# Performance work log

Hardware: AMD Instinct MI355X
Metric: run time of the kernel (lower is better)

Reference implementation:

```python
import jax, jax.numpy as jnp
import numpy as np

W, B, S, D = 4, 1, 1024, 1024   # simulated world_size, batch, local seq, embed_dim
H, DS, HM = 16, 64, 4            # num_heads, summary_dim, meta_heads


def mha(q, k, v, w_in, b_in, w_out, b_out, nheads):
    """torch nn.MultiheadAttention (batch_first). Returns (out, head-averaged weights)."""
    d = q.shape[-1]
    hd = d // nheads
    wq, wk, wv = jnp.split(w_in, 3, axis=0)
    bq, bk, bv = jnp.split(b_in, 3)
    Bq, Sq, _ = q.shape
    Sk = k.shape[1]
    qh = (q @ wq.T + bq).reshape(Bq, Sq, nheads, hd)
    kh = (k @ wk.T + bk).reshape(Bq, Sk, nheads, hd)
    vh = (v @ wv.T + bv).reshape(Bq, Sk, nheads, hd)
    scores = jnp.einsum('bqhd,bkhd->bhqk', qh, kh) / float(np.sqrt(hd))
    attn = jax.nn.softmax(scores, axis=-1)
    out = jnp.einsum('bhqk,bkhd->bqhd', attn, vh).reshape(Bq, Sq, d)
    return out @ w_out.T + b_out, attn.mean(axis=1)


def attn_stats(attn):
    """attn: (B, S) -> (B, 4) [entropy, gini, max, top5]."""
    ent = -(attn * jnp.log(attn + 1e-8)).sum(-1, keepdims=True)
    s = jnp.sort(attn, axis=-1)
    n = attn.shape[-1]
    idx = jnp.arange(1, n + 1, dtype=attn.dtype)
    gini = 2.0 * (idx * s).sum(-1) / (n * s.sum(-1) + 1e-8) - (n + 1) / n
    mx = attn.max(-1, keepdims=True)
    k = min(5, n)
    top5 = jax.lax.top_k(attn, k)[0].sum(-1, keepdims=True)
    return jnp.concatenate([ent, gini[..., None], mx, top5], axis=-1)


def _forward(x, local_in_w, local_in_b, local_out_w, local_out_b,
             sum_query, sum_in_w, sum_in_b, sum_out_w, sum_out_b,
             pat_w1, pat_b1, pat_w2, pat_b2, comb_w, comb_b,
             meta_in_w, meta_in_b, meta_out_w, meta_out_b,
             route_w1, route_b1, route_w2, route_b2,
             cross_in_w, cross_in_b, cross_out_w, cross_out_b,
             gate_w, gate_b, proj_w, proj_b):
    nW = x.shape[0]

    # 1) local attention per rank: (W,B,S,D)
    local = jax.vmap(lambda xc: mha(xc, xc, xc, local_in_w, local_in_b,
                                    local_out_w, local_out_b, H)[0])(x)

    # 2) chunk summary per rank
    def summarize(lo):
        q = jnp.broadcast_to(sum_query, (lo.shape[0], 1, lo.shape[-1]))
        content, w = mha(q, lo, lo, sum_in_w, sum_in_b, sum_out_w, sum_out_b, H)
        content, w = content[:, 0], w[:, 0]              # (B,D), (B,S)
        pat = attn_stats(w)                               # (B,4)
        pat = jax.nn.relu(pat @ pat_w1.T + pat_b1) @ pat_w2.T + pat_b2
        return jnp.concatenate([content, pat], axis=-1) @ comb_w.T + comb_b

    summaries = jax.vmap(summarize)(local)                # (W,B,DS)
    all_sum = jnp.transpose(summaries, (1, 0, 2))         # (B,W,DS) = all-gather

    # 3) meta attention over chunk summaries -> routing weights
    refined, chunk_attn = mha(all_sum, all_sum, all_sum,
                              meta_in_w, meta_in_b, meta_out_w, meta_out_b, HM)
    logits = (jax.nn.relu(refined @ route_w1.T + route_b1) @ route_w2.T + route_b2)[..., 0]
    routing = jax.nn.softmax(logits, axis=-1)             # (B,W)

    all_chunks = jnp.transpose(local, (1, 0, 2, 3))       # (B,W,S,D) = all-gather

    # 4) selective cross-attention + gated combine, per rank
    def per_rank(r, lo):
        rm = routing * (1.0 - jax.nn.one_hot(r, nW, dtype=routing.dtype))
        rm = rm / (rm.sum(-1, keepdims=True) + 1e-8)
        kv = jnp.einsum('bw,bwsd->bsd', rm, all_chunks)
        cross, _ = mha(lo, kv, kv, cross_in_w, cross_in_b, cross_out_w, cross_out_b, H)
        g = jax.nn.sigmoid(jnp.concatenate([lo, cross], axis=-1) @ gate_w.T + gate_b)
        comb = g * cross + (1.0 - g) * lo
        return comb @ proj_w.T + proj_b

    out = jax.vmap(per_rank)(jnp.arange(nW), local)       # (W,B,S,D)
    return out


def setup_inputs() -> dict:
    key = jax.random.key(0)
    ks = iter(jax.random.split(key, 40))
    p = lambda *shape: jax.random.normal(next(ks), shape, dtype=jnp.float32) * 0.02
    inp = {
        'x': jax.random.normal(next(ks), (W, B, S, D), dtype=jnp.float32),
        'local_in_w': p(3 * D, D), 'local_in_b': p(3 * D),
        'local_out_w': p(D, D), 'local_out_b': p(D),
        'sum_query': p(1, 1, D),
        'sum_in_w': p(3 * D, D), 'sum_in_b': p(3 * D),
        'sum_out_w': p(D, D), 'sum_out_b': p(D),
        'pat_w1': p(DS, 4), 'pat_b1': p(DS),
        'pat_w2': p(DS, DS), 'pat_b2': p(DS),
        'comb_w': p(DS, D + DS), 'comb_b': p(DS),
        'meta_in_w': p(3 * DS, DS), 'meta_in_b': p(3 * DS),
        'meta_out_w': p(DS, DS), 'meta_out_b': p(DS),
        'route_w1': p(DS, DS), 'route_b1': p(DS),
        'route_w2': p(1, DS), 'route_b2': p(1),
        'cross_in_w': p(3 * D, D), 'cross_in_b': p(3 * D),
        'cross_out_w': p(D, D), 'cross_out_b': p(D),
        'gate_w': p(D, 2 * D), 'gate_b': p(D),
        'proj_w': p(D, D), 'proj_b': p(D),
    }
    return inp


def reference(x, local_in_w, local_in_b, local_out_w, local_out_b,
              sum_query, sum_in_w, sum_in_b, sum_out_w, sum_out_b,
              pat_w1, pat_b1, pat_w2, pat_b2, comb_w, comb_b,
              meta_in_w, meta_in_b, meta_out_w, meta_out_b,
              route_w1, route_b1, route_w2, route_b2,
              cross_in_w, cross_in_b, cross_out_w, cross_out_b,
              gate_w, gate_b, proj_w, proj_b):
    return _forward(x, local_in_w, local_in_b, local_out_w, local_out_b,
                    sum_query, sum_in_w, sum_in_b, sum_out_w, sum_out_b,
                    pat_w1, pat_b1, pat_w2, pat_b2, comb_w, comb_b,
                    meta_in_w, meta_in_b, meta_out_w, meta_out_b,
                    route_w1, route_b1, route_w2, route_b2,
                    cross_in_w, cross_in_b, cross_out_w, cross_out_b,
                    gate_w, gate_b, proj_w, proj_b)
```

## Files before the change

kernel.cpp:

```cpp
#include <hip/hip_runtime.h>
#include <stdint.h>

typedef uint16_t u16;
typedef __attribute__((ext_vector_type(8))) short short8;
typedef __attribute__((ext_vector_type(8))) unsigned short ushort8;
typedef __attribute__((ext_vector_type(4))) float f32x4;

#define AS1 __attribute__((address_space(1)))
#define AS3 __attribute__((address_space(3)))

__device__ __forceinline__ float b2f(u16 u){
  union{uint32_t i; float f;} v; v.i=((uint32_t)u)<<16; return v.f;
}
__device__ __forceinline__ u16 f2b(float f){
  union{uint32_t i; float f;} v; v.f=f;
  return (u16)((v.i + 0x7fffu + ((v.i>>16)&1u))>>16);
}

struct CvtP { const float* src[8]; u16* dst[8]; long n[8]; };
__global__ void cvt_multi(CvtP p) {
  const int seg = blockIdx.y;
  const long i = ((long)blockIdx.x*256 + threadIdx.x)*8;
  if (i >= p.n[seg]) return;
  const float* in = p.src[seg];
  float4 a = *(const float4*)&in[i];
  float4 b = *(const float4*)&in[i+4];
  ushort8 o;
  o[0]=f2b(a.x); o[1]=f2b(a.y); o[2]=f2b(a.z); o[3]=f2b(a.w);
  o[4]=f2b(b.x); o[5]=f2b(b.y); o[6]=f2b(b.z); o[7]=f2b(b.w);
  *(ushort8*)&p.dst[seg][i] = o;
}

struct GemmP {
  const u16* A; const u16* B; u16* C; const float* bias;
  const u16* B2; u16* C2; const float* bias2;
  long lda, ldb, ldc, ldb2, ldc2;
  int K, Nstore, Nstore2, ySplit, act, outf;
  float scale;
};

__global__ __launch_bounds__(512) void gemm_nt(GemmP p) {
  __shared__ __align__(16) u16 lA[2][4096];
  __shared__ __align__(16) u16 lB[2][4096];
  const int t = threadIdx.x;
  const int wave = t >> 6, lane = t & 63;
  int by = blockIdx.y;
  const u16* Bp; u16* Cp; const float* bias; long ldb, ldc; int nst;
  if (by >= p.ySplit) {
    by -= p.ySplit; Bp = p.B2; Cp = p.C2; bias = p.bias2;
    ldb = p.ldb2; ldc = p.ldc2; nst = p.Nstore2;
  } else {
    Bp = p.B; Cp = p.C; bias = p.bias; ldb = p.ldb; ldc = p.ldc; nst = p.Nstore;
  }
  const u16* A = p.A + (long)blockIdx.x * 128 * p.lda;
  const u16* B = Bp + (long)by * 128 * ldb;
  const int srow = t >> 2, skk = (t & 3) * 8;
  const int wr = wave >> 2, wc = wave & 3;
  const int fr = lane & 15, fk = (lane >> 4) * 8;
  f32x4 acc[4][2] = {};

  __builtin_amdgcn_global_load_lds((const AS1 void*)(A + (long)srow*p.lda + skk),
                                   (AS3 void*)&lA[0][t*8], 16, 0, 0);
  __builtin_amdgcn_global_load_lds((const AS1 void*)(B + (long)srow*ldb + skk),
                                   (AS3 void*)&lB[0][t*8], 16, 0, 0);
  __syncthreads();
  int cur = 0;
  for (int k0 = 0; k0 < p.K; k0 += 32) {
    if (k0 + 32 < p.K) {
      const int nb = cur ^ 1, kn = k0 + 32;
      __builtin_amdgcn_global_load_lds((const AS1 void*)(A + (long)srow*p.lda + kn + skk),
                                       (AS3 void*)&lA[nb][t*8], 16, 0, 0);
      __builtin_amdgcn_global_load_lds((const AS1 void*)(B + (long)srow*ldb + kn + skk),
                                       (AS3 void*)&lB[nb][t*8], 16, 0, 0);
    }
    short8 av[4], bv[2];
    #pragma unroll
    for (int mi = 0; mi < 4; ++mi) av[mi] = *(const short8*)&lA[cur][(wr*64 + mi*16 + fr)*32 + fk];
    #pragma unroll
    for (int ni = 0; ni < 2; ++ni) bv[ni] = *(const short8*)&lB[cur][(wc*32 + ni*16 + fr)*32 + fk];
    #pragma unroll
    for (int mi = 0; mi < 4; ++mi)
      #pragma unroll
      for (int ni = 0; ni < 2; ++ni)
        acc[mi][ni] = __builtin_amdgcn_mfma_f32_16x16x32_bf16(av[mi], bv[ni], acc[mi][ni], 0, 0, 0);
    __syncthreads();
    cur ^= 1;
  }

  const int rbase = blockIdx.x*128 + wr*64;
  const int cbase = by*128 + wc*32;
  const int rsub = (lane >> 4) * 4;
  #pragma unroll
  for (int ni = 0; ni < 2; ++ni) {
    const int col = cbase + ni*16 + fr;
    if (col >= nst) continue;
    const float bs = bias ? bias[col] : 0.f;
    #pragma unroll
    for (int mi = 0; mi < 4; ++mi) {
      #pragma unroll
      for (int j = 0; j < 4; ++j) {
        float v = acc[mi][ni][j] * p.scale + bs;
        if (p.act == 1) v = 1.f / (1.f + __expf(-v));
        const long idx = (long)(rbase + mi*16 + rsub + j) * ldc + col;
        if (p.outf) ((float*)Cp)[idx] = v;
        else        Cp[idx] = f2b(v);
      }
    }
  }
}

struct FlashP {
  const u16 *q, *k, *v; u16* o;
  long ldq, ldkv, ldo;
  long qB, kvB, oB;
};

__global__ __launch_bounds__(256) void flash_k(FlashP p) {
  const int t = threadIdx.x, w4 = t >> 6, lane = t & 63;
  const int qt = blockIdx.x, h = blockIdx.y, wz = blockIdx.z;
  const int fr = lane & 15, g = lane >> 4, fk = g * 8;
  __shared__ __align__(16) u16 kt[64][72];
  __shared__ __align__(16) u16 vt[64][72];
  __shared__ __align__(16) u16 pl[4][32][72];

  const u16* Q = p.q + (long)wz*p.qB + (long)(qt*128 + w4*32)*p.ldq + h*64;
  const u16* K = p.k + (long)wz*p.kvB + h*64;
  const u16* V = p.v + (long)wz*p.kvB + h*64;

  short8 aq[2][2];
  #pragma unroll
  for (int mi = 0; mi < 2; ++mi)
    #pragma unroll
    for (int ks = 0; ks < 2; ++ks)
      aq[mi][ks] = *(const short8*)&Q[(long)(mi*16 + fr)*p.ldq + ks*32 + fk];

  f32x4 acc[2][4] = {};
  float mst[2][4], lst[2][4];
  #pragma unroll
  for (int mi = 0; mi < 2; ++mi)
    #pragma unroll
    for (int j = 0; j < 4; ++j) { mst[mi][j] = -3e38f; lst[mi][j] = 0.f; }

  const int srow = t >> 2, sseg = (t & 3) * 16;

  for (int k0 = 0; k0 < 1024; k0 += 64) {
    {
      const u16* Kr = K + (long)(k0 + srow)*p.ldkv + sseg;
      const u16* Vr = V + (long)(k0 + srow)*p.ldkv + sseg;
      *(short8*)&kt[srow][sseg]     = *(const short8*)Kr;
      *(short8*)&kt[srow][sseg + 8] = *(const short8*)(Kr + 8);
      ushort8 v0 = *(const ushort8*)Vr;
      ushort8 v1 = *(const ushort8*)(Vr + 8);
      #pragma unroll
      for (int e = 0; e < 8; ++e) {
        vt[sseg + e][srow]     = v0[e];
        vt[sseg + 8 + e][srow] = v1[e];
      }
    }
    __syncthreads();

    f32x4 s[2][4] = {};
    #pragma unroll
    for (int ni = 0; ni < 4; ++ni) {
      short8 bk0 = *(const short8*)&kt[ni*16 + fr][fk];
      short8 bk1 = *(const short8*)&kt[ni*16 + fr][32 + fk];
      #pragma unroll
      for (int mi = 0; mi < 2; ++mi) {
        s[mi][ni] = __builtin_amdgcn_mfma_f32_16x16x32_bf16(aq[mi][0], bk0, s[mi][ni], 0, 0, 0);
        s[mi][ni] = __builtin_amdgcn_mfma_f32_16x16x32_bf16(aq[mi][1], bk1, s[mi][ni], 0, 0, 0);
      }
    }
    #pragma unroll
    for (int mi = 0; mi < 2; ++mi)
      #pragma unroll
      for (int ni = 0; ni < 4; ++ni) s[mi][ni] *= 0.125f;

    #pragma unroll
    for (int mi = 0; mi < 2; ++mi) {
      #pragma unroll
      for (int j = 0; j < 4; ++j) {
        float rm = -3e38f;
        #pragma unroll
        for (int ni = 0; ni < 4; ++ni) rm = fmaxf(rm, s[mi][ni][j]);
        #pragma unroll
        for (int o = 8; o; o >>= 1) rm = fmaxf(rm, __shfl_xor(rm, o, 64));
        const float mnew = fmaxf(mst[mi][j], rm);
        const float alpha = __expf(mst[mi][j] - mnew);
        float rs = 0.f;
        #pragma unroll
        for (int ni = 0; ni < 4; ++ni) {
          const float pv = __expf(s[mi][ni][j] - mnew);
          s[mi][ni][j] = pv;
          rs += pv;
        }
        #pragma unroll
        for (int o = 8; o; o >>= 1) rs += __shfl_xor(rs, o, 64);
        lst[mi][j] = lst[mi][j]*alpha + rs;
        mst[mi][j] = mnew;
        #pragma unroll
        for (int ni = 0; ni < 4; ++ni) acc[mi][ni][j] *= alpha;
      }
    }

    #pragma unroll
    for (int mi = 0; mi < 2; ++mi)
      #pragma unroll
      for (int ni = 0; ni < 4; ++ni)
        #pragma unroll
        for (int j = 0; j < 4; ++j)
          pl[w4][mi*16 + g*4 + j][ni*16 + fr] = f2b(s[mi][ni][j]);

    #pragma unroll
    for (int ks = 0; ks < 2; ++ks) {
      short8 pa0 = *(const short8*)&pl[w4][fr][ks*32 + fk];
      short8 pa1 = *(const short8*)&pl[w4][16 + fr][ks*32 + fk];
      #pragma unroll
      for (int nv = 0; nv < 4; ++nv) {
        short8 bvv = *(const short8*)&vt[nv*16 + fr][ks*32 + fk];
        acc[0][nv] = __builtin_amdgcn_mfma_f32_16x16x32_bf16(pa0, bvv, acc[0][nv], 0, 0, 0);
        acc[1][nv] = __builtin_amdgcn_mfma_f32_16x16x32_bf16(pa1, bvv, acc[1][nv], 0, 0, 0);
      }
    }
    __syncthreads();
  }

  u16* O = p.o + (long)wz*p.oB + (long)(qt*128 + w4*32)*p.ldo + h*64;
  #pragma unroll
  for (int mi = 0; mi < 2; ++mi) {
    #pragma unroll
    for (int j = 0; j < 4; ++j) {
      const float inv = 1.f / lst[mi][j];
      #pragma unroll
      for (int nv = 0; nv < 4; ++nv)
        O[(long)(mi*16 + g*4 + j)*p.ldo + nv*16 + fr] = f2b(acc[mi][nv][j] * inv);
    }
  }
}

__global__ void gemv_qs(const float* sq, const float* w, const float* b, float* out) {
  const int t = threadIdx.x, nl = t & 63, kq = t >> 6;
  const int n = blockIdx.x*64 + nl;
  const float* row = w + (long)n * 1024 + kq*256;
  const float* q = sq + kq*256;
  float s = 0.f;
  for (int k = 0; k < 256; k += 4) {
    float4 ww = *(const float4*)&row[k];
    float4 qq = *(const float4*)&q[k];
    s += qq.x*ww.x + qq.y*ww.y + qq.z*ww.z + qq.w*ww.w;
  }
  __shared__ float ps[4][64];
  ps[kq][nl] = s;
  __syncthreads();
  if (t < 64) out[blockIdx.x*64 + t] = ps[0][t]+ps[1][t]+ps[2][t]+ps[3][t] + b[blockIdx.x*64 + t];
}

__global__ void sum_attend(const float* qs, const u16* sumkv, float* content, float* pall) {
  const int h = blockIdx.x, w = blockIdx.y, t = threadIdx.x;
  const int lane = t & 63, wv = t >> 6;
  __shared__ float qsh[64];
  __shared__ float sc[1024];
  __shared__ float rmax[4], rsum[4];
  __shared__ float po[4][64];
  if (t < 64) qsh[t] = qs[h*64 + t];
  __syncthreads();
  const u16* kbase = sumkv + (long)w*2097152 + h*64;
  float e[4];
  float mx = -1e30f;
  #pragma unroll
  for (int j = 0; j < 4; ++j) {
    const int k = j*256 + t;
    const u16* krow = kbase + (long)k * 2048;
    float s = 0.f;
    #pragma unroll
    for (int d = 0; d < 64; d += 8) {
      ushort8 kk = *(const ushort8*)&krow[d];
      #pragma unroll
      for (int q = 0; q < 8; ++q) s += qsh[d+q] * b2f(kk[q]);
    }
    s *= 0.125f;
    e[j] = s;
    mx = fmaxf(mx, s);
  }
  #pragma unroll
  for (int o = 32; o; o >>= 1) mx = fmaxf(mx, __shfl_xor(mx, o, 64));
  if (lane == 0) rmax[wv] = mx;
  __syncthreads();
  mx = fmaxf(fmaxf(rmax[0],rmax[1]), fmaxf(rmax[2],rmax[3]));
  float sum = 0.f;
  #pragma unroll
  for (int j = 0; j < 4; ++j) { e[j] = __expf(e[j]-mx); sum += e[j]; }
  #pragma unroll
  for (int o = 32; o; o >>= 1) sum += __shfl_xor(sum, o, 64);
  if (lane == 0) rsum[wv] = sum;
  __syncthreads();
  const float inv = 1.f / (rsum[0]+rsum[1]+rsum[2]+rsum[3]);
  float* pr = pall + ((long)w*16 + h)*1024;
  #pragma unroll
  for (int j = 0; j < 4; ++j) {
    const int k = j*256 + t;
    const float pn = e[j]*inv;
    sc[k] = pn;
    pr[k] = pn;
  }
  __syncthreads();
  const u16* vbase = sumkv + (long)w*2097152 + 1024 + h*64;
  float o = 0.f;
  const int k0 = wv*256;
  for (int k = k0; k < k0+256; ++k) o += sc[k] * b2f(vbase[(long)k*2048 + lane]);
  po[wv][lane] = o;
  __syncthreads();
  if (t < 64) content[(long)w*1024 + h*64 + t] = po[0][t]+po[1][t]+po[2][t]+po[3][t];
}

__global__ void wavg_k(const float* pall, float* wavg) {
  const int w = blockIdx.y, k = blockIdx.x*256 + threadIdx.x;
  float s = 0.f;
  #pragma unroll
  for (int h = 0; h < 16; ++h) s += pall[((long)w*16 + h)*1024 + k];
  wavg[w*1024 + k] = s * (1.f/16.f);
}

__global__ void contproj_k(const float* content, const float* w_, const float* b, float* out) {
  const int w = blockIdx.y, t = threadIdx.x;
  const int nl = t & 63, kq = t >> 6;
  const int n = blockIdx.x*64 + nl;
  const float* c = content + w*1024 + kq*256;
  const float* row = w_ + (long)n * 1024 + kq*256;
  float s = 0.f;
  for (int k = 0; k < 256; k += 4) {
    float4 ww = *(const float4*)&row[k];
    s += c[k]*ww.x + c[k+1]*ww.y + c[k+2]*ww.z + c[k+3]*ww.w;
  }
  __shared__ float ps[4][64];
  ps[kq][nl] = s;
  __syncthreads();
  if (t < 64) out[w*1024 + blockIdx.x*64 + t] = ps[0][t]+ps[1][t]+ps[2][t]+ps[3][t] + b[blockIdx.x*64 + t];
}

__global__ void stats1_k(const float* wavg, float* part) {
  const int c = blockIdx.x, w = blockIdx.y, t = threadIdx.x;
  __shared__ float a[1024];
  for (int i = t; i < 1024; i += 256) a[i] = wavg[w*1024 + i];
  __syncthreads();
  const int jl = t & 63, iq = t >> 6;
  const int j = c*64 + jl;
  const float aj = a[j];
  int pr = 0;
  const int i0 = iq*256;
  #pragma unroll 8
  for (int i = i0; i < i0+256; ++i) {
    const float ai = a[i];
    pr += (ai < aj) || (ai == aj && i < j);
  }
  __shared__ int prs[4][64];
  prs[iq][jl] = pr;
  __syncthreads();
  if (t < 64) {
    const int rank = 1 + prs[0][jl] + prs[1][jl] + prs[2][jl] + prs[3][jl];
    float ent = -aj * logf(aj + 1e-8f);
    float gnum = (float)rank * aj;
    float ssum = aj;
    float mx = aj;
    float top5 = (rank >= 1020) ? aj : 0.f;
    #pragma unroll
    for (int o = 32; o; o >>= 1) {
      ent += __shfl_xor(ent, o, 64);
      gnum += __shfl_xor(gnum, o, 64);
      ssum += __shfl_xor(ssum, o, 64);
      mx = fmaxf(mx, __shfl_xor(mx, o, 64));
      top5 += __shfl_xor(top5, o, 64);
    }
    if (t == 0) {
      float* pp = part + ((w*16 + c) * 5);
      pp[0]=ent; pp[1]=gnum; pp[2]=ssum; pp[3]=mx; pp[4]=top5;
    }
  }
}

__global__ void stats2_k(const float* part, float* stats) {
  const int w = blockIdx.x, t = threadIdx.x;
  const int c = t & 15, stat = t >> 4;
  float v = 0.f;
  const bool active = stat < 5;
  if (active) v = part[(w*16 + c)*5 + stat];
  #pragma unroll
  for (int o = 8; o; o >>= 1) {
    const float ov = __shfl_xor(v, o, 64);
    v = (stat == 3) ? fmaxf(v, ov) : (v + ov);
  }
  __shared__ float r5[5];
  if (active && c == 0) r5[stat] = v;
  __syncthreads();
  if (t == 0) {
    stats[w*4+0] = r5[0];
    stats[w*4+1] = 2.f*r5[1]/(1024.f*r5[2] + 1e-8f) - 1025.f/1024.f;
    stats[w*4+2] = r5[3];
    stats[w*4+3] = r5[4];
  }
}

__global__ void patsum_k(const float* stats, const float* contprj,
                         const float* pw1, const float* pb1, const float* pw2, const float* pb2,
                         const float* combw, const float* combb, float* summ) {
  const int w = blockIdx.x, t = threadIdx.x;
  const int nl = t & 63, kq = t >> 6;
  __shared__ float p1[64], pat[64];
  __shared__ float ps[4][64];
  __shared__ float ps2[4][64];
  if (t < 64) {
    float s = 0.f;
    #pragma unroll
    for (int k = 0; k < 4; ++k) s += stats[w*4+k] * pw1[t*4+k];
    p1[t] = fmaxf(s + pb1[t], 0.f);
  }
  __syncthreads();
  {
    float s = 0.f;
    const float* rw = pw2 + (long)nl*64 + kq*16;
    const float* pp = p1 + kq*16;
    #pragma unroll
    for (int k = 0; k < 16; ++k) s += pp[k] * rw[k];
    ps[kq][nl] = s;
  }
  __syncthreads();
  if (t < 64) pat[t] = ps[0][t]+ps[1][t]+ps[2][t]+ps[3][t] + pb2[t];
  __syncthreads();
  const float* c = contprj + w*1024;
  const float* row = combw + (long)nl * 1088;
  float s = 0.f;
  const int k0 = kq*272;
  for (int k = k0; k < k0+272; ++k) {
    const float rv = row[k];
    const float cv = (k < 1024) ? c[k] : pat[k-1024];
    s += cv * rv;
  }
  ps2[kq][nl] = s;
  __syncthreads();
  if (t < 64) summ[w*64 + t] = ps2[0][t]+ps2[1][t]+ps2[2][t]+ps2[3][t] + combb[t];
}

__global__ void meta_k(const float* summ, const float* miw, const float* mib,
                       const float* mow, const float* mob, const float* rw1, const float* rb1,
                       const float* rw2, const float* rb2, float* routing) {
  const int t = threadIdx.x;
  __shared__ float qkv[4][192];
  __shared__ float sc[64];
  __shared__ float o[4][64];
  __shared__ float rf[4][64];
  __shared__ float t1[4][64];
  __shared__ float lg[4];
  for (int idx = t; idx < 768; idx += 64) {
    const int w = idx / 192, rrow = idx % 192;
    const float* rw = miw + (long)rrow * 64;
    float s = 0.f;
    for (int k = 0; k < 64; ++k) s += summ[w*64+k] * rw[k];
    qkv[w][rrow] = s + mib[rrow];
  }
  __syncthreads();
  {
    const int h = t >> 4, i = (t >> 2) & 3, j = t & 3;
    float s = 0.f;
    #pragma unroll
    for (int d = 0; d < 16; ++d) s += qkv[i][h*16+d] * qkv[j][64 + h*16+d];
    sc[t] = s * 0.25f;
  }
  __syncthreads();
  if (t < 16) {
    const float a0=sc[t*4], a1=sc[t*4+1], a2=sc[t*4+2], a3=sc[t*4+3];
    const float m = fmaxf(fmaxf(a0,a1), fmaxf(a2,a3));
    const float e0=__expf(a0-m), e1=__expf(a1-m), e2=__expf(a2-m), e3=__expf(a3-m);
    const float s = e0+e1+e2+e3;
    sc[t*4]=e0/s; sc[t*4+1]=e1/s; sc[t*4+2]=e2/s; sc[t*4+3]=e3/s;
  }
  __syncthreads();
  for (int idx = t; idx < 256; idx += 64) {
    const int i = idx >> 6, c = idx & 63, h = c >> 4;
    float s = 0.f;
    #pragma unroll
    for (int j = 0; j < 4; ++j) s += sc[(h*4+i)*4+j] * qkv[j][128 + c];
    o[i][c] = s;
  }
  __syncthreads();
  for (int idx = t; idx < 256; idx += 64) {
    const int i = idx >> 6, n = idx & 63;
    const float* rw = mow + (long)n * 64;
    float s = 0.f;
    for (int k = 0; k < 64; ++k) s += o[i][k] * rw[k];
    rf[i][n] = s + mob[n];
  }
  __syncthreads();
  for (int idx = t; idx < 256; idx += 64) {
    const int i = idx >> 6, n = idx & 63;
    const float* rw = rw1 + (long)n * 64;
    float s = 0.f;
    for (int k = 0; k < 64; ++k) s += rf[i][k] * rw[k];
    t1[i][n] = fmaxf(s + rb1[n], 0.f);
  }
  __syncthreads();
  if (t < 4) {
    float s = 0.f;
    for (int k = 0; k < 64; ++k) s += t1[t][k] * rw2[k];
    lg[t] = s + rb2[0];
  }
  __syncthreads();
  if (t == 0) {
    const float m = fmaxf(fmaxf(lg[0],lg[1]), fmaxf(lg[2],lg[3]));
    float e[4], s = 0.f;
    #pragma unroll
    for (int i = 0; i < 4; ++i) { e[i] = __expf(lg[i]-m); s += e[i]; }
    #pragma unroll
    for (int i = 0; i < 4; ++i) routing[i] = e[i]/s;
  }
}

__global__ void kvr_k(const u16* local, const float* routing, u16* kvr) {
  const int r = blockIdx.y;
  const long e = ((long)blockIdx.x*256 + threadIdx.x) * 8;
  float rm[4]; float s = 0.f;
  #pragma unroll
  for (int w = 0; w < 4; ++w) { rm[w] = (w == r) ? 0.f : routing[w]; s += rm[w]; }
  const float inv = 1.f / (s + 1e-8f);
  ushort8 a0 = *(const ushort8*)&local[e];
  ushort8 a1 = *(const ushort8*)&local[1048576 + e];
  ushort8 a2 = *(const ushort8*)&local[2097152 + e];
  ushort8 a3 = *(const ushort8*)&local[3145728 + e];
  ushort8 out;
  #pragma unroll
  for (int j = 0; j < 8; ++j)
    out[j] = f2b((rm[0]*b2f(a0[j]) + rm[1]*b2f(a1[j]) + rm[2]*b2f(a2[j]) + rm[3]*b2f(a3[j])) * inv);
  *(ushort8*)&kvr[(long)r*1048576 + e] = out;
}

__global__ void gcat_k(const u16* local, const u16* cross, u16* gcat) {
  const long e = ((long)blockIdx.x*256 + threadIdx.x) * 8;
  const long row = e >> 11, col = e & 2047;
  const u16* src = (col < 1024) ? &local[row*1024 + col] : &cross[row*1024 + col - 1024];
  *(ushort8*)&gcat[e] = *(const ushort8*)src;
}

__global__ void comb_k(const u16* g, const u16* cross, const u16* local, u16* comb) {
  const long e = ((long)blockIdx.x*256 + threadIdx.x) * 8;
  ushort8 gg = *(const ushort8*)&g[e];
  ushort8 cc = *(const ushort8*)&cross[e];
  ushort8 ll = *(const ushort8*)&local[e];
  ushort8 out;
  #pragma unroll
  for (int j = 0; j < 8; ++j) {
    const float gf = b2f(gg[j]);
    out[j] = f2b(gf*b2f(cc[j]) + (1.f-gf)*b2f(ll[j]));
  }
  *(ushort8*)&comb[e] = out;
}

static void gemm1(hipStream_t st, dim3 grid,
                  const u16* A, long lda, const u16* B, long ldb,
                  u16* C, long ldc, const float* bias,
                  int K, int N, float scale, int act, int outf) {
  GemmP p = {};
  p.A=A; p.B=B; p.C=C; p.bias=bias;
  p.lda=lda; p.ldb=ldb; p.ldc=ldc;
  p.K=K; p.Nstore=N; p.ySplit=1<<30; p.act=act; p.outf=outf; p.scale=scale;
  gemm_nt<<<grid, dim3(512), 0, st>>>(p);
}

extern "C" void kernel_launch(void* const* d_in, const int* in_sizes, int n_in,
                              void* d_out, int out_size, void* d_ws, size_t ws_size,
                              hipStream_t stream) {
  (void)in_sizes; (void)n_in; (void)out_size; (void)ws_size;
  const float* x   = (const float*)d_in[0];
  const float* liw = (const float*)d_in[1];
  const float* lib = (const float*)d_in[2];
  const float* low = (const float*)d_in[3];
  const float* lob = (const float*)d_in[4];
  const float* sq  = (const float*)d_in[5];
  const float* siw = (const float*)d_in[6];
  const float* sib = (const float*)d_in[7];
  const float* sow = (const float*)d_in[8];
  const float* sob = (const float*)d_in[9];
  const float* pw1 = (const float*)d_in[10];
  const float* pb1 = (const float*)d_in[11];
  const float* pw2 = (const float*)d_in[12];
  const float* pb2 = (const float*)d_in[13];
  const float* cbw = (const float*)d_in[14];
  const float* cbb = (const float*)d_in[15];
  const float* miw = (const float*)d_in[16];
  const float* mib = (const float*)d_in[17];
  const float* mow = (const float*)d_in[18];
  const float* mob = (const float*)d_in[19];
  const float* rw1 = (const float*)d_in[20];
  const float* rb1 = (const float*)d_in[21];
  const float* rw2 = (const float*)d_in[22];
  const float* rb2 = (const float*)d_in[23];
  const float* ciw = (const float*)d_in[24];
  const float* cib = (const float*)d_in[25];
  const float* cow = (const float*)d_in[26];
  const float* cob = (const float*)d_in[27];
  const float* gw  = (const float*)d_in[28];
  const float* gb  = (const float*)d_in[29];
  const float* pw  = (const float*)d_in[30];
  const float* pb  = (const float*)d_in[31];

  char* ws = (char*)d_ws;
  u16* qkv    = (u16*)(ws + 0);
  u16* aout   = (u16*)(ws + 25165824);
  u16* local  = (u16*)(ws + 33554432);
  u16* scratch= (u16*)(ws + 41943040);
  u16* s2048  = (u16*)(ws + 79691776);
  u16* cq     = (u16*)(ws + 96468992);
  u16* kvr    = (u16*)(ws + 104857600);
  u16* crossb = (u16*)(ws + 113246208);
  char* sf = ws + 121634816;
  float* qs      = (float*)(sf + 0);
  float* pall    = (float*)(sf + 4096);
  float* wavg    = (float*)(sf + 266240);
  float* content = (float*)(sf + 282624);
  float* contprj = (float*)(sf + 299008);
  float* stats   = (float*)(sf + 315392);
  float* summ    = (float*)(sf + 315456);
  float* routing = (float*)(sf + 316480);
  float* part    = (float*)(sf + 316544);
  u16* siwkvb = (u16*)(ws + 122028032);
  u16* lowb   = (u16*)(ws + 126222336);
  u16* ciwb   = (u16*)(ws + 128319488);
  u16* cowb   = (u16*)(ws + 134610944);
  u16* gwb    = (u16*)(ws + 136708096);
  u16* pwb    = (u16*)(ws + 140902400);
  u16* xb   = crossb;
  u16* liwb = scratch;

  CvtP cp;
  cp.src[0]=x;   cp.dst[0]=xb;     cp.n[0]=4194304;
  cp.src[1]=liw; cp.dst[1]=liwb;   cp.n[1]=3145728;
  cp.src[2]=low; cp.dst[2]=lowb;   cp.n[2]=1048576;
  cp.src[3]=siw+1048576; cp.dst[3]=siwkvb; cp.n[3]=2097152;
  cp.src[4]=ciw; cp.dst[4]=ciwb;   cp.n[4]=3145728;
  cp.src[5]=cow; cp.dst[5]=cowb;   cp.n[5]=1048576;
  cp.src[6]=gw;  cp.dst[6]=gwb;    cp.n[6]=2097152;
  cp.src[7]=pw;  cp.dst[7]=pwb;    cp.n[7]=1048576;
  cvt_multi<<<dim3(2048, 8), dim3(256), 0, stream>>>(cp);

  gemm1(stream, dim3(32,24), xb,1024, liwb,1024, qkv,3072, lib, 1024, 3072, 1.f, 0, 0);

  {
    FlashP fp;
    fp.q = qkv; fp.k = qkv + 1024; fp.v = qkv + 2048; fp.o = aout;
    fp.ldq = 3072; fp.ldkv = 3072; fp.ldo = 1024;
    fp.qB = 3145728; fp.kvB = 3145728; fp.oB = 1048576;
    flash_k<<<dim3(8,16,4), dim3(256), 0, stream>>>(fp);
  }

  gemm1(stream, dim3(32,8), aout,1024, lowb,1024, local,1024, lob, 1024, 1024, 1.f, 0, 0);

  {
    GemmP p = {};
    p.A = local; p.lda = 1024; p.K = 1024; p.scale = 1.f;
    p.B = ciwb;   p.C = cq;    p.bias = cib;      p.ldb = 1024; p.ldc = 1024; p.Nstore = 1024;
    p.B2 = siwkvb; p.C2 = s2048; p.bias2 = sib+1024; p.ldb2 = 1024; p.ldc2 = 2048; p.Nstore2 = 2048;
    p.ySplit = 8;
    gemm_nt<<<dim3(32,24), dim3(512), 0, stream>>>(p);
  }

  gemv_qs<<<dim3(16), dim3(256), 0, stream>>>(sq, siw, sib, qs);
  sum_attend<<<dim3(16,4), dim3(256), 0, stream>>>(qs, s2048, content, pall);
  wavg_k<<<dim3(4,4), dim3(256), 0, stream>>>(pall, wavg);
  contproj_k<<<dim3(16,4), dim3(256), 0, stream>>>(content, sow, sob, contprj);
  stats1_k<<<dim3(16,4), dim3(256), 0, stream>>>(wavg, part);
  stats2_k<<<dim3(4), dim3(128), 0, stream>>>(part, stats);
  patsum_k<<<dim3(4), dim3(256), 0, stream>>>(stats, contprj, pw1, pb1, pw2, pb2, cbw, cbb, summ);

  meta_k<<<dim3(1), dim3(64), 0, stream>>>(summ, miw, mib, mow, mob, rw1, rb1, rw2, rb2, routing);

  kvr_k<<<dim3(512,4), dim3(256), 0, stream>>>(local, routing, kvr);

  gemm1(stream, dim3(32,16), kvr,1024, ciwb+1048576,1024, s2048,2048, cib+1024, 1024, 2048, 1.f, 0, 0);

  {
    FlashP fp;
    fp.q = cq; fp.k = s2048; fp.v = s2048 + 1024; fp.o = aout;
    fp.ldq = 1024; fp.ldkv = 2048; fp.ldo = 1024;
    fp.qB = 1048576; fp.kvB = 2097152; fp.oB = 1048576;
    flash_k<<<dim3(8,16,4), dim3(256), 0, stream>>>(fp);
  }

  gemm1(stream, dim3(32,8), aout,1024, cowb,1024, crossb,1024, cob, 1024, 1024, 1.f, 0, 0);

  gcat_k<<<dim3(4096), dim3(256), 0, stream>>>(local, crossb, s2048);
  gemm1(stream, dim3(32,8), s2048,2048, gwb,2048, cq,1024, gb, 2048, 1024, 1.f, 1, 0);

  comb_k<<<dim3(2048), dim3(256), 0, stream>>>(cq, crossb, local, kvr);

  gemm1(stream, dim3(32,8), kvr,1024, pwb,1024, (u16*)d_out,1024, pb, 1024, 1024, 1.f, 0, 1);
}
```

Before: 498.4 us.

## Restructure flash attention: smaller Q tiles, register-prefetched K/V, packed V transpose

The flash attention kernel now gives each wave 16 query rows instead of 32, so the grid doubles to 16 query tiles per head. This raises the block count for occupancy, but each block reloads the full K/V. The next K/V tile is prefetched into registers while the current one is computed, and the V transpose into shared memory writes packed 32-bit pairs instead of single 16-bit stores. It also adds s_setprio around the MFMA sections and uses the HIP bf16 conversion intrinsic in place of the manual rounding.

```diff
diff --git a/kernel.cpp b/kernel.cpp
--- a/kernel.cpp
+++ b/kernel.cpp
@@ -1,4 +1,5 @@
 #include <hip/hip_runtime.h>
+#include <hip/hip_bf16.h>
 #include <stdint.h>
 
 typedef uint16_t u16;
@@ -15,6 +16,10 @@
 __device__ __forceinline__ u16 f2b(float f){
   union{uint32_t i; float f;} v; v.f=f;
   return (u16)((v.i + 0x7fffu + ((v.i>>16)&1u))>>16);
+}
+__device__ __forceinline__ u16 f2bf(float f){
+  __hip_bfloat16 h = __float2bfloat16(f);
+  return *reinterpret_cast<u16*>(&h);
 }
 
 struct CvtP { const float* src[8]; u16* dst[8]; long n[8]; };
@@ -121,119 +126,110 @@
   const int fr = lane & 15, g = lane >> 4, fk = g * 8;
   __shared__ __align__(16) u16 kt[64][72];
   __shared__ __align__(16) u16 vt[64][72];
-  __shared__ __align__(16) u16 pl[4][32][72];
-
-  const u16* Q = p.q + (long)wz*p.qB + (long)(qt*128 + w4*32)*p.ldq + h*64;
+  __shared__ __align__(16) u16 pl[4][16][72];
+
+  const u16* Q = p.q + (long)wz*p.qB + (long)(qt*64 + w4*16)*p.ldq + h*64;
   const u16* K = p.k + (long)wz*p.kvB + h*64;
   const u16* V = p.v + (long)wz*p.kvB + h*64;
 
-  short8 aq[2][2];
-  #pragma unroll
-  for (int mi = 0; mi < 2; ++mi)
-    #pragma unroll
-    for (int ks = 0; ks < 2; ++ks)
-      aq[mi][ks] = *(const short8*)&Q[(long)(mi*16 + fr)*p.ldq + ks*32 + fk];
-
-  f32x4 acc[2][4] = {};
-  float mst[2][4], lst[2][4];
-  #pragma unroll
-  for (int mi = 0; mi < 2; ++mi)
-    #pragma unroll
-    for (int j = 0; j < 4; ++j) { mst[mi][j] = -3e38f; lst[mi][j] = 0.f; }
-
-  const int srow = t >> 2, sseg = (t & 3) * 16;
-
-  for (int k0 = 0; k0 < 1024; k0 += 64) {
-    {
-      const u16* Kr = K + (long)(k0 + srow)*p.ldkv + sseg;
-      const u16* Vr = V + (long)(k0 + srow)*p.ldkv + sseg;
-      *(short8*)&kt[srow][sseg]     = *(const short8*)Kr;
-      *(short8*)&kt[srow][sseg + 8] = *(const short8*)(Kr + 8);
-      ushort8 v0 = *(const ushort8*)Vr;
-      ushort8 v1 = *(const ushort8*)(Vr + 8);
-      #pragma unroll
-      for (int e = 0; e < 8; ++e) {
-        vt[sseg + e][srow]     = v0[e];
-        vt[sseg + 8 + e][srow] = v1[e];
-      }
+  short8 aq[2];
+  aq[0] = *(const short8*)&Q[(long)fr*p.ldq + fk];
+  aq[1] = *(const short8*)&Q[(long)fr*p.ldq + 32 + fk];
+
+  f32x4 acc[4] = {};
+  float mst[4], lst[4];
+  #pragma unroll
+  for (int j = 0; j < 4; ++j) { mst[j] = -3e38f; lst[j] = 0.f; }
+
+  const int krow = t >> 2, kseg = (t & 3) * 16;
+  const int vp = t & 31, vc = (t >> 5) * 8;
+
+  short8 kr0, kr1, vr0, vr1;
+  kr0 = *(const short8*)&K[(long)krow*p.ldkv + kseg];
+  kr1 = *(const short8*)&K[(long)krow*p.ldkv + kseg + 8];
+  vr0 = *(const short8*)&V[(long)(2*vp)*p.ldkv + vc];
+  vr1 = *(const short8*)&V[(long)(2*vp + 1)*p.ldkv + vc];
+
+  for (int it = 0; it < 16; ++it) {
+    *(short8*)&kt[krow][kseg]     = kr0;
+    *(short8*)&kt[krow][kseg + 8] = kr1;
+    #pragma unroll
+    for (int e = 0; e < 8; ++e) {
+      const uint32_t pk = (uint32_t)(uint16_t)vr0[e] | ((uint32_t)(uint16_t)vr1[e] << 16);
+      *(uint32_t*)&vt[vc + e][2*vp] = pk;
     }
     __syncthreads();
 
-    f32x4 s[2][4] = {};
+    if (it + 1 < 16) {
+      const int kn = (it + 1) * 64;
+      kr0 = *(const short8*)&K[(long)(kn + krow)*p.ldkv + kseg];
+      kr1 = *(const short8*)&K[(long)(kn + krow)*p.ldkv + kseg + 8];
+      vr0 = *(const short8*)&V[(long)(kn + 2*vp)*p.ldkv + vc];
+      vr1 = *(const short8*)&V[(long)(kn + 2*vp + 1)*p.ldkv + vc];
+    }
+
+    f32x4 s[4] = {};
+    __builtin_amdgcn_s_setprio(1);
     #pragma unroll
     for (int ni = 0; ni < 4; ++ni) {
       short8 bk0 = *(const short8*)&kt[ni*16 + fr][fk];
       short8 bk1 = *(const short8*)&kt[ni*16 + fr][32 + fk];
-      #pragma unroll
-      for (int mi = 0; mi < 2; ++mi) {
-        s[mi][ni] = __builtin_amdgcn_mfma_f32_16x16x32_bf16(aq[mi][0], bk0, s[mi][ni], 0, 0, 0);
-        s[mi][ni] = __builtin_amdgcn_mfma_f32_16x16x32_bf16(aq[mi][1], bk1, s[mi][ni], 0, 0, 0);
+      s[ni] = __builtin_amdgcn_mfma_f32_16x16x32_bf16(aq[0], bk0, s[ni], 0, 0, 0);
+      s[ni] = __builtin_amdgcn_mfma_f32_16x16x32_bf16(aq[1], bk1, s[ni], 0, 0, 0);
+    }
+    __builtin_amdgcn_s_setprio(0);
+    #pragma unroll
+    for (int ni = 0; ni < 4; ++ni) s[ni] *= 0.125f;
+
+    #pragma unroll
+    for (int j = 0; j < 4; ++j) {
+      float rm = fmaxf(fmaxf(s[0][j], s[1][j]), fmaxf(s[2][j], s[3][j]));
+      #pragma unroll
+      for (int o = 8; o; o >>= 1) rm = fmaxf(rm, __shfl_xor(rm, o, 64));
+      const float mnew = fmaxf(mst[j], rm);
+      const float alpha = __expf(mst[j] - mnew);
+      float rs = 0.f;
+      #pragma unroll
+      for (int ni = 0; ni < 4; ++ni) {
+        const float pv = __expf(s[ni][j] - mnew);
+        s[ni][j] = pv;
+        rs += pv;
       }
-    }
-    #pragma unroll
-    for (int mi = 0; mi < 2; ++mi)
-      #pragma unroll
-      for (int ni = 0; ni < 4; ++ni) s[mi][ni] *= 0.125f;
-
-    #pragma unroll
-    for (int mi = 0; mi < 2; ++mi) {
-      #pragma unroll
-      for (int j = 0; j < 4; ++j) {
-        float rm = -3e38f;
-        #pragma unroll
-        for (int ni = 0; ni < 4; ++ni) rm = fmaxf(rm, s[mi][ni][j]);
-        #pragma unroll
-        for (int o = 8; o; o >>= 1) rm = fmaxf(rm, __shfl_xor(rm, o, 64));
-        const float mnew = fmaxf(mst[mi][j], rm);
-        const float alpha = __expf(mst[mi][j] - mnew);
-        float rs = 0.f;
-        #pragma unroll
-        for (int ni = 0; ni < 4; ++ni) {
-          const float pv = __expf(s[mi][ni][j] - mnew);
-          s[mi][ni][j] = pv;
-          rs += pv;
-        }
-        #pragma unroll
-        for (int o = 8; o; o >>= 1) rs += __shfl_xor(rs, o, 64);
-        lst[mi][j] = lst[mi][j]*alpha + rs;
-        mst[mi][j] = mnew;
-        #pragma unroll
-        for (int ni = 0; ni < 4; ++ni) acc[mi][ni][j] *= alpha;
-      }
-    }
-
-    #pragma unroll
-    for (int mi = 0; mi < 2; ++mi)
-      #pragma unroll
-      for (int ni = 0; ni < 4; ++ni)
-        #pragma unroll
-        for (int j = 0; j < 4; ++j)
-          pl[w4][mi*16 + g*4 + j][ni*16 + fr] = f2b(s[mi][ni][j]);
-
+      #pragma unroll
+      for (int o = 8; o; o >>= 1) rs += __shfl_xor(rs, o, 64);
+      lst[j] = lst[j]*alpha + rs;
+      mst[j] = mnew;
+      #pragma unroll
+      for (int nv = 0; nv < 4; ++nv) acc[nv][j] *= alpha;
+    }
+
+    #pragma unroll
+    for (int ni = 0; ni < 4; ++ni)
+      #pragma unroll
+      for (int j = 0; j < 4; ++j)
+        pl[w4][g*4 + j][ni*16 + fr] = f2bf(s[ni][j]);
+
+    __builtin_amdgcn_s_setprio(1);
     #pragma unroll
     for (int ks = 0; ks < 2; ++ks) {
-      short8 pa0 = *(const short8*)&pl[w4][fr][ks*32 + fk];
-      short8 pa1 = *(const short8*)&pl[w4][16 + fr][ks*32 + fk];
+      short8 pa = *(const short8*)&pl[w4][fr][ks*32 + fk];
       #pragma unroll
       for (int nv = 0; nv < 4; ++nv) {
         short8 bvv = *(const short8*)&vt[nv*16 + fr][ks*32 + fk];
-        acc[0][nv] = __builtin_amdgcn_mfma_f32_16x16x32_bf16(pa0, bvv, acc[0][nv], 0, 0, 0);
-        acc[1][nv] = __builtin_amdgcn_mfma_f32_16x16x32_bf16(pa1, bvv, acc[1][nv], 0, 0, 0);
+        acc[nv] = __builtin_amdgcn_mfma_f32_16x16x32_bf16(pa, bvv, acc[nv], 0, 0, 0);
       }
     }
+    __builtin_amdgcn_s_setprio(0);
     __syncthreads();
   }
 
-  u16* O = p.o + (long)wz*p.oB + (long)(qt*128 + w4*32)*p.ldo + h*64;
-  #pragma unroll
-  for (int mi = 0; mi < 2; ++mi) {
-    #pragma unroll
-    for (int j = 0; j < 4; ++j) {
-      const float inv = 1.f / lst[mi][j];
-      #pragma unroll
-      for (int nv = 0; nv < 4; ++nv)
-        O[(long)(mi*16 + g*4 + j)*p.ldo + nv*16 + fr] = f2b(acc[mi][nv][j] * inv);
-    }
+  u16* O = p.o + (long)wz*p.oB + (long)(qt*64 + w4*16)*p.ldo + h*64;
+  #pragma unroll
+  for (int j = 0; j < 4; ++j) {
+    const float inv = 1.f / lst[j];
+    #pragma unroll
+    for (int nv = 0; nv < 4; ++nv)
+      O[(long)(g*4 + j)*p.ldo + nv*16 + fr] = f2bf(acc[nv][j] * inv);
   }
 }
 
@@ -646,7 +642,7 @@
     fp.q = qkv; fp.k = qkv + 1024; fp.v = qkv + 2048; fp.o = aout;
     fp.ldq = 3072; fp.ldkv = 3072; fp.ldo = 1024;
     fp.qB = 3145728; fp.kvB = 3145728; fp.oB = 1048576;
-    flash_k<<<dim3(8,16,4), dim3(256), 0, stream>>>(fp);
+    flash_k<<<dim3(16,16,4), dim3(256), 0, stream>>>(fp);
   }
 
   gemm1(stream, dim3(32,8), aout,1024, lowb,1024, local,1024, lob, 1024, 1024, 1.f, 0, 0);
@@ -679,7 +675,7 @@
     fp.q = cq; fp.k = s2048; fp.v = s2048 + 1024; fp.o = aout;
     fp.ldq = 1024; fp.ldkv = 2048; fp.ldo = 1024;
     fp.qB = 1048576; fp.kvB = 2097152; fp.oB = 1048576;
-    flash_k<<<dim3(8,16,4), dim3(256), 0, stream>>>(fp);
+    flash_k<<<dim3(16,16,4), dim3(256), 0, stream>>>(fp);
   }
 
   gemm1(stream, dim3(32,8), aout,1024, cowb,1024, crossb,1024, cob, 1024, 1024, 1.f, 0, 0);
```

Result: faster. 463.1 us (-7.1%).
